# Optimization experiments

Hardware: AMD Instinct MI355X
Metric: run time of the kernel (lower is better)

The kernel has to match this reference:

```python
import jax, jax.numpy as jnp
import numpy as np

B, T, E, D, A, EMB, V = 128, 96, 512, 512, 512, 512, 4096


def _linear_params(k, out_d, in_d):
    bound = 1.0 / np.sqrt(in_d)
    k1, k2 = jax.random.split(k)
    W = jax.random.uniform(k1, (out_d, in_d), minval=-bound, maxval=bound)
    b = jax.random.uniform(k2, (out_d,), minval=-bound, maxval=bound)
    return W, b


def setup_inputs() -> dict:
    key = jax.random.key(0)
    ks = jax.random.split(key, 16)
    W_enc, b_enc = _linear_params(ks[0], A, E)
    W_dec, b_dec = _linear_params(ks[1], A, D)
    W_full, b_full = _linear_params(ks[2], 1, A)
    W_init_h, b_init_h = _linear_params(ks[3], D, E)
    W_init_c, b_init_c = _linear_params(ks[4], D, E)
    W_fbeta, b_fbeta = _linear_params(ks[5], E, D)
    W_fc = jax.random.uniform(ks[6], (V, D), minval=-0.1, maxval=0.1)
    b_fc = jnp.zeros((V,), jnp.float32)
    emb_table = jax.random.uniform(ks[7], (V, EMB), minval=-0.1, maxval=0.1)
    W_ih, b_ih = _linear_params(ks[8], 4 * D, EMB + E)
    W_hh, b_hh = _linear_params(ks[9], 4 * D, D)
    encoder_out = jax.random.normal(ks[10], (B, E), jnp.float32)
    encoded_captions = jax.random.randint(ks[11], (B, T), 0, V)
    caption_lengths = jax.random.randint(ks[12], (B, 1), 1, T + 1)
    return dict(encoder_out=encoder_out, encoded_captions=encoded_captions,
                caption_lengths=caption_lengths,
                W_enc=W_enc, b_enc=b_enc, W_dec=W_dec, b_dec=b_dec,
                W_full=W_full, b_full=b_full,
                W_init_h=W_init_h, b_init_h=b_init_h,
                W_init_c=W_init_c, b_init_c=b_init_c,
                W_fbeta=W_fbeta, b_fbeta=b_fbeta,
                W_fc=W_fc, b_fc=b_fc, emb_table=emb_table,
                W_ih=W_ih, b_ih=b_ih, W_hh=W_hh, b_hh=b_hh)


def reference(encoder_out, encoded_captions, caption_lengths,
              W_enc, b_enc, W_dec, b_dec, W_full, b_full,
              W_init_h, b_init_h, W_init_c, b_init_c,
              W_fbeta, b_fbeta, W_fc, b_fc, emb_table,
              W_ih, b_ih, W_hh, b_hh):
    # sort by caption length, descending (as in torch forward)
    lens = caption_lengths[:, 0]
    order = jnp.argsort(-lens)
    enc = encoder_out[order]            # (B, E)
    caps = encoded_captions[order]      # (B, T)
    lens_s = lens[order]
    embeds = emb_table[caps]            # (B, T, EMB)
    h0 = enc @ W_init_h.T + b_init_h    # (B, D)
    c0 = enc @ W_init_c.T + b_init_c
    att1 = enc @ W_enc.T + b_enc        # (B, A), fixed over time
    # valid[t, i] == (i < batch_size_t), since lengths are sorted descending
    valid = (jnp.arange(T)[None, :] < lens_s[:, None]).T  # (T, B)

    def step(carry, xs):
        h, c = carry
        emb_t, v = xs                   # (B, EMB), (B,) bool
        att2 = h @ W_dec.T + b_dec      # (B, A)
        # additive attention over the batch dim (the actual math of My_attention on 2D input)
        scores = jax.nn.relu(att1[None, :, :] + att2[:, None, :]) @ W_full[0] + b_full[0]  # (B, B)
        scores = jnp.where(v[None, :], scores, -1e9)
        alpha = jax.nn.softmax(scores, axis=1)
        awe = alpha @ enc               # (B, E)
        gate = jax.nn.sigmoid(h @ W_fbeta.T + b_fbeta)
        awe = gate * awe
        x = jnp.concatenate([emb_t, awe], axis=1)  # (B, EMB+E)
        gates = x @ W_ih.T + b_ih + h @ W_hh.T + b_hh
        gi, gf, gg, go = jnp.split(gates, 4, axis=1)  # torch LSTMCell order: i,f,g,o
        gi, gf, go = jax.nn.sigmoid(gi), jax.nn.sigmoid(gf), jax.nn.sigmoid(go)
        gg = jnp.tanh(gg)
        c_new = gf * c + gi * gg
        h_new = go * jnp.tanh(c_new)
        preds = h_new @ W_fc.T + b_fc   # dropout is identity in eval
        vm = v[:, None]
        return (jnp.where(vm, h_new, h), jnp.where(vm, c_new, c)), jnp.where(vm, preds, 0.0)

    (_, _), preds = jax.lax.scan(jax.checkpoint(step), (h0, c0),
                                 (jnp.transpose(embeds, (1, 0, 2)), valid))
    # (B, T, V), rows in sorted order, zero-padded past each caption length
    # (torch pack_padded_sequence is a pure reordering/gather of exactly these entries)
    return jnp.transpose(preds, (1, 0, 2))
```

## Files before the change

### kernel.cpp

```cpp
#include <hip/hip_runtime.h>

#define Bsz  128
#define Tlen 96
#define Edim 512
#define Ddim 512
#define Adim 512
#define EMBd 512
#define Vdim 4096

typedef __attribute__((ext_vector_type(8))) short short8v;
typedef __attribute__((ext_vector_type(4))) float f32x4;

__device__ __forceinline__ float sigm(float x) { return 1.0f / (1.0f + expf(-x)); }
__device__ __forceinline__ unsigned short f2bf(float f) {
    unsigned int x = __float_as_uint(f);
    unsigned int r = (x + 0x7FFFu + ((x >> 16) & 1u)) >> 16;
    return (unsigned short)r;
}

__global__ void k_sort(const int* __restrict__ lens, int* __restrict__ order,
                       int* __restrict__ lens_s) {
    __shared__ int L[Bsz];
    int j = threadIdx.x;
    L[j] = lens[j];
    __syncthreads();
    int lj = L[j];
    int rank = 0;
    for (int m = 0; m < Bsz; ++m) {
        int lm = L[m];
        if (lm > lj || (lm == lj && m < j)) rank++;
    }
    order[rank] = j;
    lens_s[rank] = lj;
}

__global__ void k_gather(const float* __restrict__ enc_in,
                         const int* __restrict__ order, float* __restrict__ enc_s) {
    int i = blockIdx.x;
    int src = order[i];
    for (int d = threadIdx.x; d < Edim; d += 256)
        enc_s[i * Edim + d] = enc_in[src * Edim + d];
}

__global__ void k_cvtW(const float* __restrict__ W, unsigned short* __restrict__ O,
                       int n) {
    int i = blockIdx.x * 256 + threadIdx.x;
    if (i < n) O[i] = f2bf(W[i]);
}

__device__ __forceinline__ void mm_tile(const float* __restrict__ act,
                                        const float* __restrict__ W,
                                        int K, int i0, float acc[4][4]) {
    __shared__ float sA[64][17];
    __shared__ float sB[64][17];
    int tid = threadIdx.x;
    int tx = tid & 15, ty = tid >> 4;
    for (int k0 = 0; k0 < K; k0 += 16) {
        {
            int idx = tid * 4;
            int row = idx >> 4;
            int kk = idx & 15;
            const float* p = act + (size_t)(i0 + row) * K + k0 + kk;
            float4 v = *reinterpret_cast<const float4*>(p);
            sA[row][kk + 0] = v.x; sA[row][kk + 1] = v.y;
            sA[row][kk + 2] = v.z; sA[row][kk + 3] = v.w;
        }
        {
            int idx = tid * 4;
            int row = idx >> 4;
            int kk = idx & 15;
            const float* p = W + (size_t)row * K + k0 + kk;
            float4 v = *reinterpret_cast<const float4*>(p);
            sB[row][kk + 0] = v.x; sB[row][kk + 1] = v.y;
            sB[row][kk + 2] = v.z; sB[row][kk + 3] = v.w;
        }
        __syncthreads();
#pragma unroll
        for (int kk = 0; kk < 16; ++kk) {
            float a[4], b[4];
#pragma unroll
            for (int r = 0; r < 4; ++r) a[r] = sA[ty * 4 + r][kk];
#pragma unroll
            for (int cidx = 0; cidx < 4; ++cidx) b[cidx] = sB[tx * 4 + cidx][kk];
#pragma unroll
            for (int r = 0; r < 4; ++r)
#pragma unroll
                for (int cidx = 0; cidx < 4; ++cidx)
                    acc[r][cidx] += a[r] * b[cidx];
        }
        __syncthreads();
    }
}

__global__ __launch_bounds__(256) void k_init(
    const float* __restrict__ enc_s,
    const float* __restrict__ W_init_h, const float* __restrict__ b_init_h,
    const float* __restrict__ W_init_c, const float* __restrict__ b_init_c,
    const float* __restrict__ W_enc, const float* __restrict__ b_enc,
    float* __restrict__ h, float* __restrict__ c, float* __restrict__ att1) {
    int j0 = blockIdx.x * 64;
    int i0 = blockIdx.y * 64;
    const float* W; const float* bias; float* out; int jl;
    if (j0 < 512)       { W = W_init_h; bias = b_init_h; out = h;    jl = j0; }
    else if (j0 < 1024) { W = W_init_c; bias = b_init_c; out = c;    jl = j0 - 512; }
    else                { W = W_enc;    bias = b_enc;    out = att1; jl = j0 - 1024; }
    float acc[4][4] = {};
    mm_tile(enc_s, W + (size_t)jl * Edim, Edim, i0, acc);
    int tx = threadIdx.x & 15, ty = threadIdx.x >> 4;
#pragma unroll
    for (int r = 0; r < 4; ++r)
#pragma unroll
        for (int cc = 0; cc < 4; ++cc) {
            int i = i0 + ty * 4 + r, j = jl + tx * 4 + cc;
            out[i * 512 + j] = acc[r][cc] + bias[j];
        }
}

__global__ __launch_bounds__(256) void k_stepA(
    const float* __restrict__ h,
    const float* __restrict__ W_dec, const float* __restrict__ b_dec,
    const float* __restrict__ W_fbeta, const float* __restrict__ b_fbeta,
    const float* __restrict__ W_hh, const float* __restrict__ b_hh,
    float* __restrict__ att2, float* __restrict__ gate, float* __restrict__ hh) {
    int j0 = blockIdx.x * 64;
    int i0 = blockIdx.y * 64;
    int tx = threadIdx.x & 15, ty = threadIdx.x >> 4;
    if (j0 < 512) {
        float acc[4][4] = {};
        mm_tile(h, W_dec + (size_t)j0 * Ddim, Ddim, i0, acc);
#pragma unroll
        for (int r = 0; r < 4; ++r)
#pragma unroll
            for (int cc = 0; cc < 4; ++cc) {
                int i = i0 + ty * 4 + r, j = j0 + tx * 4 + cc;
                att2[i * 512 + j] = acc[r][cc] + b_dec[j];
            }
    } else if (j0 < 1024) {
        float acc[4][4] = {};
        int jl = j0 - 512;
        mm_tile(h, W_fbeta + (size_t)jl * Ddim, Ddim, i0, acc);
#pragma unroll
        for (int r = 0; r < 4; ++r)
#pragma unroll
            for (int cc = 0; cc < 4; ++cc) {
                int i = i0 + ty * 4 + r, j = jl + tx * 4 + cc;
                gate[i * 512 + j] = sigm(acc[r][cc] + b_fbeta[j]);
            }
    } else {
        float acc[4][4] = {};
        int jl = j0 - 1024;
        mm_tile(h, W_hh + (size_t)jl * Ddim, Ddim, i0, acc);
#pragma unroll
        for (int r = 0; r < 4; ++r)
#pragma unroll
            for (int cc = 0; cc < 4; ++cc) {
                int i = i0 + ty * 4 + r, j = jl + tx * 4 + cc;
                hh[i * 2048 + j] = acc[r][cc] + b_hh[j];
            }
    }
}

__global__ __launch_bounds__(256) void k_stepB(
    const float* __restrict__ att1, const float* __restrict__ att2,
    const float* __restrict__ enc_s,
    const float* __restrict__ W_full, const float* __restrict__ b_full,
    const float* __restrict__ gate, const float* __restrict__ emb_table,
    const int* __restrict__ caps, const int* __restrict__ order,
    const int* __restrict__ lens_s, float* __restrict__ x, int t) {
    int i = blockIdx.x;
    int tid = threadIdx.x;
    __shared__ float sA2[512];
    __shared__ float sWF[512];
    __shared__ float sSC[128];
    __shared__ float sRed[2];
    for (int d = tid; d < 512; d += 256) {
        sA2[d] = att2[i * 512 + d];
        sWF[d] = W_full[d];
    }
    __syncthreads();
    if (tid < 128) {
        int j = tid;
        const float* a1 = att1 + j * 512;
        float acc = 0.0f;
        for (int k = 0; k < 512; ++k) {
            float v = a1[k] + sA2[k];
            acc += fmaxf(v, 0.0f) * sWF[k];
        }
        float sc = acc + b_full[0];
        if (t >= lens_s[j]) sc = -1000000000.0f;
        sSC[j] = sc;
    }
    __syncthreads();
    if (tid < 64) {
        float m = fmaxf(sSC[tid], sSC[tid + 64]);
        for (int o = 32; o; o >>= 1) m = fmaxf(m, __shfl_down(m, o));
        if (tid == 0) sRed[0] = m;
    }
    __syncthreads();
    if (tid < 128) sSC[tid] = expf(sSC[tid] - sRed[0]);
    __syncthreads();
    if (tid < 64) {
        float s = sSC[tid] + sSC[tid + 64];
        for (int o = 32; o; o >>= 1) s += __shfl_down(s, o);
        if (tid == 0) sRed[1] = s;
    }
    __syncthreads();
    float inv = 1.0f / sRed[1];
    int cap = caps[order[i] * Tlen + t];
    for (int d = tid; d < 512; d += 256) {
        float acc = 0.0f;
        for (int j = 0; j < 128; ++j) acc += sSC[j] * enc_s[j * 512 + d];
        acc *= inv;
        x[i * 1024 + 512 + d] = gate[i * 512 + d] * acc;
        x[i * 1024 + d] = emb_table[(size_t)cap * EMBd + d];
    }
}

__global__ __launch_bounds__(256) void k_stepC(
    const float* __restrict__ x, const float* __restrict__ W_ih,
    const float* __restrict__ b_ih, const float* __restrict__ hh,
    float* __restrict__ gates) {
    int j0 = blockIdx.x * 64;
    int i0 = blockIdx.y * 64;
    float acc[4][4] = {};
    mm_tile(x, W_ih + (size_t)j0 * 1024, 1024, i0, acc);
    int tx = threadIdx.x & 15, ty = threadIdx.x >> 4;
#pragma unroll
    for (int r = 0; r < 4; ++r)
#pragma unroll
        for (int cc = 0; cc < 4; ++cc) {
            int i = i0 + ty * 4 + r, j = j0 + tx * 4 + cc;
            gates[i * 2048 + j] = acc[r][cc] + b_ih[j] + hh[i * 2048 + j];
        }
}

__global__ void k_lstm(const float* __restrict__ gates, float* __restrict__ h,
                       float* __restrict__ c, const int* __restrict__ lens_s,
                       unsigned short* __restrict__ h_hist, int t) {
    int idx = blockIdx.x * 256 + threadIdx.x;
    int i = idx >> 9, d = idx & 511;
    float hv;
    if (t < lens_s[i]) {
        float gi = sigm(gates[i * 2048 + d]);
        float gf = sigm(gates[i * 2048 + 512 + d]);
        float gg = tanhf(gates[i * 2048 + 1024 + d]);
        float go = sigm(gates[i * 2048 + 1536 + d]);
        float cn = gf * c[idx] + gi * gg;
        hv = go * tanhf(cn);
        c[idx] = cn;
        h[idx] = hv;
    } else {
        hv = h[idx];
    }
    h_hist[(size_t)t * (Bsz * 512) + idx] = f2bf(hv);
}

__global__ __launch_bounds__(256) void k_preds(
    const unsigned short* __restrict__ hh16, const unsigned short* __restrict__ wfc16,
    const float* __restrict__ b_fc, const int* __restrict__ lens_s,
    float* __restrict__ out) {
    int nb = blockIdx.x;
    int mb = blockIdx.y;
    int wid = threadIdx.x >> 6;
    int lane = threadIdx.x & 63;
    int wr = wid >> 1, wc = wid & 1;
    int m_wave = mb * 128 + wr * 64;
    int n_wave = nb * 128 + wc * 64;
    int r = lane & 15, g = lane >> 4;
    f32x4 acc[4][4];
#pragma unroll
    for (int a = 0; a < 4; ++a)
#pragma unroll
        for (int b = 0; b < 4; ++b) acc[a][b] = (f32x4){0.f, 0.f, 0.f, 0.f};
    for (int kk = 0; kk < 512; kk += 32) {
        short8v av[4], bv[4];
#pragma unroll
        for (int mf = 0; mf < 4; ++mf)
            av[mf] = *reinterpret_cast<const short8v*>(
                &hh16[(size_t)(m_wave + mf * 16 + r) * 512 + kk + g * 8]);
#pragma unroll
        for (int nf = 0; nf < 4; ++nf)
            bv[nf] = *reinterpret_cast<const short8v*>(
                &wfc16[(size_t)(n_wave + nf * 16 + r) * 512 + kk + g * 8]);
#pragma unroll
        for (int mf = 0; mf < 4; ++mf)
#pragma unroll
            for (int nf = 0; nf < 4; ++nf)
                acc[mf][nf] = __builtin_amdgcn_mfma_f32_16x16x32_bf16(
                    av[mf], bv[nf], acc[mf][nf], 0, 0, 0);
    }
#pragma unroll
    for (int mf = 0; mf < 4; ++mf)
#pragma unroll
        for (int nf = 0; nf < 4; ++nf)
#pragma unroll
            for (int reg = 0; reg < 4; ++reg) {
                int m = m_wave + mf * 16 + g * 4 + reg;
                int col = n_wave + nf * 16 + r;
                int t = m >> 7, i = m & 127;
                bool valid = t < lens_s[i];
                out[((size_t)i * Tlen + t) * Vdim + col] =
                    valid ? acc[mf][nf][reg] + b_fc[col] : 0.0f;
            }
}

extern "C" void kernel_launch(void* const* d_in, const int* in_sizes, int n_in,
                              void* d_out, int out_size, void* d_ws, size_t ws_size,
                              hipStream_t stream) {
    const float* encoder_out = (const float*)d_in[0];
    const int* caps = (const int*)d_in[1];
    const int* lens = (const int*)d_in[2];
    const float* W_enc = (const float*)d_in[3];
    const float* b_enc = (const float*)d_in[4];
    const float* W_dec = (const float*)d_in[5];
    const float* b_dec = (const float*)d_in[6];
    const float* W_full = (const float*)d_in[7];
    const float* b_full = (const float*)d_in[8];
    const float* W_init_h = (const float*)d_in[9];
    const float* b_init_h = (const float*)d_in[10];
    const float* W_init_c = (const float*)d_in[11];
    const float* b_init_c = (const float*)d_in[12];
    const float* W_fbeta = (const float*)d_in[13];
    const float* b_fbeta = (const float*)d_in[14];
    const float* W_fc = (const float*)d_in[15];
    const float* b_fc = (const float*)d_in[16];
    const float* emb_table = (const float*)d_in[17];
    const float* W_ih = (const float*)d_in[18];
    const float* b_ih = (const float*)d_in[19];
    const float* W_hh = (const float*)d_in[20];
    const float* b_hh = (const float*)d_in[21];
    float* out = (float*)d_out;

    char* p = (char*)d_ws;
    auto alloc = [&](size_t bytes) {
        void* r = (void*)p;
        p += (bytes + 255) & ~(size_t)255;
        return r;
    };
    int* order = (int*)alloc(Bsz * 4);
    int* lens_s = (int*)alloc(Bsz * 4);
    float* enc_s = (float*)alloc(Bsz * Edim * 4);
    float* att1 = (float*)alloc(Bsz * Adim * 4);
    float* h = (float*)alloc(Bsz * Ddim * 4);
    float* c = (float*)alloc(Bsz * Ddim * 4);
    float* att2 = (float*)alloc(Bsz * Adim * 4);
    float* gate = (float*)alloc(Bsz * Ddim * 4);
    float* hh = (float*)alloc(Bsz * 2048 * 4);
    float* x = (float*)alloc(Bsz * 1024 * 4);
    float* gates = (float*)alloc(Bsz * 2048 * 4);
    unsigned short* h_hist = (unsigned short*)alloc((size_t)Tlen * Bsz * 512 * 2);
    unsigned short* wfc16 = (unsigned short*)alloc((size_t)Vdim * Ddim * 2);

    k_sort<<<1, 128, 0, stream>>>(lens, order, lens_s);
    k_gather<<<Bsz, 256, 0, stream>>>(encoder_out, order, enc_s);
    k_cvtW<<<(Vdim * Ddim + 255) / 256, 256, 0, stream>>>(W_fc, wfc16, Vdim * Ddim);
    k_init<<<dim3(24, 2), 256, 0, stream>>>(enc_s, W_init_h, b_init_h, W_init_c,
                                            b_init_c, W_enc, b_enc, h, c, att1);
    for (int t = 0; t < Tlen; ++t) {
        k_stepA<<<dim3(48, 2), 256, 0, stream>>>(h, W_dec, b_dec, W_fbeta, b_fbeta,
                                                 W_hh, b_hh, att2, gate, hh);
        k_stepB<<<Bsz, 256, 0, stream>>>(att1, att2, enc_s, W_full, b_full, gate,
                                         emb_table, caps, order, lens_s, x, t);
        k_stepC<<<dim3(32, 2), 256, 0, stream>>>(x, W_ih, b_ih, hh, gates);
        k_lstm<<<256, 256, 0, stream>>>(gates, h, c, lens_s, h_hist, t);
    }
    k_preds<<<dim3(32, 96), 256, 0, stream>>>(h_hist, wfc16, b_fc, lens_s, out);
}
```

Before: 13.23 ms.

## Fuse per-timestep kernels into one persistent kernel with grid barriers

Replaces the four kernel launches per timestep (384 launches in total) with a single persistent kernel of 128 blocks that loops over all timesteps. The stages are separated by an atomic-counter grid barrier that is reset in the sort kernel. This removes launch overhead and the inter-kernel gaps on the serial recurrence. In exchange, some blocks sit idle during the matmul phases, and correctness depends on all 128 blocks being resident at the same time.

```diff
diff --git a/kernel.cpp b/kernel.cpp
--- a/kernel.cpp
+++ b/kernel.cpp
@@ -19,9 +19,10 @@
 }
 
 __global__ void k_sort(const int* __restrict__ lens, int* __restrict__ order,
-                       int* __restrict__ lens_s) {
+                       int* __restrict__ lens_s, unsigned int* __restrict__ bar) {
     __shared__ int L[Bsz];
     int j = threadIdx.x;
+    if (j == 0) bar[0] = 0u;
     L[j] = lens[j];
     __syncthreads();
     int lj = L[j];
@@ -116,143 +117,169 @@
         }
 }
 
-__global__ __launch_bounds__(256) void k_stepA(
-    const float* __restrict__ h,
-    const float* __restrict__ W_dec, const float* __restrict__ b_dec,
-    const float* __restrict__ W_fbeta, const float* __restrict__ b_fbeta,
-    const float* __restrict__ W_hh, const float* __restrict__ b_hh,
-    float* __restrict__ att2, float* __restrict__ gate, float* __restrict__ hh) {
-    int j0 = blockIdx.x * 64;
-    int i0 = blockIdx.y * 64;
-    int tx = threadIdx.x & 15, ty = threadIdx.x >> 4;
-    if (j0 < 512) {
-        float acc[4][4] = {};
-        mm_tile(h, W_dec + (size_t)j0 * Ddim, Ddim, i0, acc);
-#pragma unroll
-        for (int r = 0; r < 4; ++r)
-#pragma unroll
-            for (int cc = 0; cc < 4; ++cc) {
-                int i = i0 + ty * 4 + r, j = j0 + tx * 4 + cc;
-                att2[i * 512 + j] = acc[r][cc] + b_dec[j];
-            }
-    } else if (j0 < 1024) {
-        float acc[4][4] = {};
-        int jl = j0 - 512;
-        mm_tile(h, W_fbeta + (size_t)jl * Ddim, Ddim, i0, acc);
-#pragma unroll
-        for (int r = 0; r < 4; ++r)
-#pragma unroll
-            for (int cc = 0; cc < 4; ++cc) {
-                int i = i0 + ty * 4 + r, j = jl + tx * 4 + cc;
-                gate[i * 512 + j] = sigm(acc[r][cc] + b_fbeta[j]);
-            }
-    } else {
-        float acc[4][4] = {};
-        int jl = j0 - 1024;
-        mm_tile(h, W_hh + (size_t)jl * Ddim, Ddim, i0, acc);
-#pragma unroll
-        for (int r = 0; r < 4; ++r)
-#pragma unroll
-            for (int cc = 0; cc < 4; ++cc) {
-                int i = i0 + ty * 4 + r, j = jl + tx * 4 + cc;
-                hh[i * 2048 + j] = acc[r][cc] + b_hh[j];
-            }
+#define NBLK 128
+__device__ __forceinline__ void gbar(unsigned int* bar, unsigned int target) {
+    __syncthreads();
+    if (threadIdx.x == 0) {
+        __threadfence();
+        __hip_atomic_fetch_add(bar, 1u, __ATOMIC_RELEASE, __HIP_MEMORY_SCOPE_AGENT);
+        while (__hip_atomic_load(bar, __ATOMIC_ACQUIRE, __HIP_MEMORY_SCOPE_AGENT)
+               < target)
+            __builtin_amdgcn_s_sleep(1);
+        __threadfence();
     }
-}
-
-__global__ __launch_bounds__(256) void k_stepB(
-    const float* __restrict__ att1, const float* __restrict__ att2,
-    const float* __restrict__ enc_s,
-    const float* __restrict__ W_full, const float* __restrict__ b_full,
-    const float* __restrict__ gate, const float* __restrict__ emb_table,
-    const int* __restrict__ caps, const int* __restrict__ order,
-    const int* __restrict__ lens_s, float* __restrict__ x, int t) {
-    int i = blockIdx.x;
+    __syncthreads();
+}
+
+struct LoopArgs {
+    const float* att1; const float* enc_s;
+    const float* W_dec; const float* b_dec;
+    const float* W_fbeta; const float* b_fbeta;
+    const float* W_hh; const float* b_hh;
+    const float* W_full; const float* b_full;
+    const float* emb_table;
+    const int* caps; const int* order; const int* lens_s;
+    const float* W_ih; const float* b_ih;
+    float* h; float* c; float* att2; float* gate; float* hh;
+    float* x; float* gates;
+    unsigned short* h_hist;
+    unsigned int* bar;
+};
+
+__global__ __launch_bounds__(256) void k_loop(LoopArgs A) {
+    int bid = blockIdx.x;
     int tid = threadIdx.x;
+    unsigned int barno = 0;
+    __shared__ float sWF[512];
     __shared__ float sA2[512];
-    __shared__ float sWF[512];
     __shared__ float sSC[128];
     __shared__ float sRed[2];
-    for (int d = tid; d < 512; d += 256) {
-        sA2[d] = att2[i * 512 + d];
-        sWF[d] = W_full[d];
+    for (int d = tid; d < 512; d += 256) sWF[d] = A.W_full[d];
+    float bfull = A.b_full[0];
+
+    for (int t = 0; t < Tlen; ++t) {
+        if (bid < 96) {
+            int j0 = (bid >> 1) * 64;
+            int i0 = (bid & 1) * 64;
+            int tx = tid & 15, ty = tid >> 4;
+            if (j0 < 512) {
+                float acc[4][4] = {};
+                mm_tile(A.h, A.W_dec + (size_t)j0 * Ddim, Ddim, i0, acc);
+#pragma unroll
+                for (int r = 0; r < 4; ++r)
+#pragma unroll
+                    for (int cc = 0; cc < 4; ++cc) {
+                        int i = i0 + ty * 4 + r, j = j0 + tx * 4 + cc;
+                        A.att2[i * 512 + j] = acc[r][cc] + A.b_dec[j];
+                    }
+            } else if (j0 < 1024) {
+                float acc[4][4] = {};
+                int jl = j0 - 512;
+                mm_tile(A.h, A.W_fbeta + (size_t)jl * Ddim, Ddim, i0, acc);
+#pragma unroll
+                for (int r = 0; r < 4; ++r)
+#pragma unroll
+                    for (int cc = 0; cc < 4; ++cc) {
+                        int i = i0 + ty * 4 + r, j = jl + tx * 4 + cc;
+                        A.gate[i * 512 + j] = sigm(acc[r][cc] + A.b_fbeta[j]);
+                    }
+            } else {
+                float acc[4][4] = {};
+                int jl = j0 - 1024;
+                mm_tile(A.h, A.W_hh + (size_t)jl * Ddim, Ddim, i0, acc);
+#pragma unroll
+                for (int r = 0; r < 4; ++r)
+#pragma unroll
+                    for (int cc = 0; cc < 4; ++cc) {
+                        int i = i0 + ty * 4 + r, j = jl + tx * 4 + cc;
+                        A.hh[i * 2048 + j] = acc[r][cc] + A.b_hh[j];
+                    }
+            }
+        }
+        gbar(A.bar, ++barno * NBLK);
+
+        {
+            int i = bid;
+            for (int d = tid; d < 512; d += 256) sA2[d] = A.att2[i * 512 + d];
+            __syncthreads();
+            if (tid < 128) {
+                int j = tid;
+                const float* a1 = A.att1 + j * 512;
+                float acc = 0.0f;
+                for (int k = 0; k < 512; ++k) {
+                    float v = a1[k] + sA2[k];
+                    acc += fmaxf(v, 0.0f) * sWF[k];
+                }
+                float sc = acc + bfull;
+                if (t >= A.lens_s[j]) sc = -1000000000.0f;
+                sSC[j] = sc;
+            }
+            __syncthreads();
+            if (tid < 64) {
+                float m = fmaxf(sSC[tid], sSC[tid + 64]);
+                for (int o = 32; o; o >>= 1) m = fmaxf(m, __shfl_down(m, o));
+                if (tid == 0) sRed[0] = m;
+            }
+            __syncthreads();
+            if (tid < 128) sSC[tid] = expf(sSC[tid] - sRed[0]);
+            __syncthreads();
+            if (tid < 64) {
+                float s = sSC[tid] + sSC[tid + 64];
+                for (int o = 32; o; o >>= 1) s += __shfl_down(s, o);
+                if (tid == 0) sRed[1] = s;
+            }
+            __syncthreads();
+            float inv = 1.0f / sRed[1];
+            int cap = A.caps[A.order[i] * Tlen + t];
+            for (int d = tid; d < 512; d += 256) {
+                float acc = 0.0f;
+                for (int j = 0; j < 128; ++j) acc += sSC[j] * A.enc_s[j * 512 + d];
+                acc *= inv;
+                A.x[i * 1024 + 512 + d] = A.gate[i * 512 + d] * acc;
+                A.x[i * 1024 + d] = A.emb_table[(size_t)cap * EMBd + d];
+            }
+        }
+        gbar(A.bar, ++barno * NBLK);
+
+        if (bid < 64) {
+            int j0 = (bid >> 1) * 64;
+            int i0 = (bid & 1) * 64;
+            float acc[4][4] = {};
+            mm_tile(A.x, A.W_ih + (size_t)j0 * 1024, 1024, i0, acc);
+            int tx = tid & 15, ty = tid >> 4;
+#pragma unroll
+            for (int r = 0; r < 4; ++r)
+#pragma unroll
+                for (int cc = 0; cc < 4; ++cc) {
+                    int i = i0 + ty * 4 + r, j = j0 + tx * 4 + cc;
+                    A.gates[i * 2048 + j] = acc[r][cc] + A.b_ih[j] + A.hh[i * 2048 + j];
+                }
+        }
+        gbar(A.bar, ++barno * NBLK);
+
+        {
+            int i = bid;
+            bool valid = t < A.lens_s[i];
+            for (int d = tid; d < 512; d += 256) {
+                int idx = i * 512 + d;
+                float hv;
+                if (valid) {
+                    float gi = sigm(A.gates[i * 2048 + d]);
+                    float gf = sigm(A.gates[i * 2048 + 512 + d]);
+                    float gg = tanhf(A.gates[i * 2048 + 1024 + d]);
+                    float go = sigm(A.gates[i * 2048 + 1536 + d]);
+                    float cn = gf * A.c[idx] + gi * gg;
+                    hv = go * tanhf(cn);
+                    A.c[idx] = cn;
+                    A.h[idx] = hv;
+                } else {
+                    hv = A.h[idx];
+                }
+                A.h_hist[(size_t)t * (Bsz * 512) + idx] = f2bf(hv);
+            }
+        }
+        gbar(A.bar, ++barno * NBLK);
     }
-    __syncthreads();
-    if (tid < 128) {
-        int j = tid;
-        const float* a1 = att1 + j * 512;
-        float acc = 0.0f;
-        for (int k = 0; k < 512; ++k) {
-            float v = a1[k] + sA2[k];
-            acc += fmaxf(v, 0.0f) * sWF[k];
-        }
-        float sc = acc + b_full[0];
-        if (t >= lens_s[j]) sc = -1000000000.0f;
-        sSC[j] = sc;
-    }
-    __syncthreads();
-    if (tid < 64) {
-        float m = fmaxf(sSC[tid], sSC[tid + 64]);
-        for (int o = 32; o; o >>= 1) m = fmaxf(m, __shfl_down(m, o));
-        if (tid == 0) sRed[0] = m;
-    }
-    __syncthreads();
-    if (tid < 128) sSC[tid] = expf(sSC[tid] - sRed[0]);
-    __syncthreads();
-    if (tid < 64) {
-        float s = sSC[tid] + sSC[tid + 64];
-        for (int o = 32; o; o >>= 1) s += __shfl_down(s, o);
-        if (tid == 0) sRed[1] = s;
-    }
-    __syncthreads();
-    float inv = 1.0f / sRed[1];
-    int cap = caps[order[i] * Tlen + t];
-    for (int d = tid; d < 512; d += 256) {
-        float acc = 0.0f;
-        for (int j = 0; j < 128; ++j) acc += sSC[j] * enc_s[j * 512 + d];
-        acc *= inv;
-        x[i * 1024 + 512 + d] = gate[i * 512 + d] * acc;
-        x[i * 1024 + d] = emb_table[(size_t)cap * EMBd + d];
-    }
-}
-
-__global__ __launch_bounds__(256) void k_stepC(
-    const float* __restrict__ x, const float* __restrict__ W_ih,
-    const float* __restrict__ b_ih, const float* __restrict__ hh,
-    float* __restrict__ gates) {
-    int j0 = blockIdx.x * 64;
-    int i0 = blockIdx.y * 64;
-    float acc[4][4] = {};
-    mm_tile(x, W_ih + (size_t)j0 * 1024, 1024, i0, acc);
-    int tx = threadIdx.x & 15, ty = threadIdx.x >> 4;
-#pragma unroll
-    for (int r = 0; r < 4; ++r)
-#pragma unroll
-        for (int cc = 0; cc < 4; ++cc) {
-            int i = i0 + ty * 4 + r, j = j0 + tx * 4 + cc;
-            gates[i * 2048 + j] = acc[r][cc] + b_ih[j] + hh[i * 2048 + j];
-        }
-}
-
-__global__ void k_lstm(const float* __restrict__ gates, float* __restrict__ h,
-                       float* __restrict__ c, const int* __restrict__ lens_s,
-                       unsigned short* __restrict__ h_hist, int t) {
-    int idx = blockIdx.x * 256 + threadIdx.x;
-    int i = idx >> 9, d = idx & 511;
-    float hv;
-    if (t < lens_s[i]) {
-        float gi = sigm(gates[i * 2048 + d]);
-        float gf = sigm(gates[i * 2048 + 512 + d]);
-        float gg = tanhf(gates[i * 2048 + 1024 + d]);
-        float go = sigm(gates[i * 2048 + 1536 + d]);
-        float cn = gf * c[idx] + gi * gg;
-        hv = go * tanhf(cn);
-        c[idx] = cn;
-        h[idx] = hv;
-    } else {
-        hv = h[idx];
-    }
-    h_hist[(size_t)t * (Bsz * 512) + idx] = f2bf(hv);
 }
 
 __global__ __launch_bounds__(256) void k_preds(
@@ -339,6 +366,7 @@
     };
     int* order = (int*)alloc(Bsz * 4);
     int* lens_s = (int*)alloc(Bsz * 4);
+    unsigned int* bar = (unsigned int*)alloc(256);
     float* enc_s = (float*)alloc(Bsz * Edim * 4);
     float* att1 = (float*)alloc(Bsz * Adim * 4);
     float* h = (float*)alloc(Bsz * Ddim * 4);
@@ -351,18 +379,26 @@
     unsigned short* h_hist = (unsigned short*)alloc((size_t)Tlen * Bsz * 512 * 2);
     unsigned short* wfc16 = (unsigned short*)alloc((size_t)Vdim * Ddim * 2);
 
-    k_sort<<<1, 128, 0, stream>>>(lens, order, lens_s);
+    k_sort<<<1, 128, 0, stream>>>(lens, order, lens_s, bar);
     k_gather<<<Bsz, 256, 0, stream>>>(encoder_out, order, enc_s);
     k_cvtW<<<(Vdim * Ddim + 255) / 256, 256, 0, stream>>>(W_fc, wfc16, Vdim * Ddim);
     k_init<<<dim3(24, 2), 256, 0, stream>>>(enc_s, W_init_h, b_init_h, W_init_c,
                                             b_init_c, W_enc, b_enc, h, c, att1);
-    for (int t = 0; t < Tlen; ++t) {
-        k_stepA<<<dim3(48, 2), 256, 0, stream>>>(h, W_dec, b_dec, W_fbeta, b_fbeta,
-                                                 W_hh, b_hh, att2, gate, hh);
-        k_stepB<<<Bsz, 256, 0, stream>>>(att1, att2, enc_s, W_full, b_full, gate,
-                                         emb_table, caps, order, lens_s, x, t);
-        k_stepC<<<dim3(32, 2), 256, 0, stream>>>(x, W_ih, b_ih, hh, gates);
-        k_lstm<<<256, 256, 0, stream>>>(gates, h, c, lens_s, h_hist, t);
-    }
+
+    LoopArgs la;
+    la.att1 = att1; la.enc_s = enc_s;
+    la.W_dec = W_dec; la.b_dec = b_dec;
+    la.W_fbeta = W_fbeta; la.b_fbeta = b_fbeta;
+    la.W_hh = W_hh; la.b_hh = b_hh;
+    la.W_full = W_full; la.b_full = b_full;
+    la.emb_table = emb_table;
+    la.caps = caps; la.order = order; la.lens_s = lens_s;
+    la.W_ih = W_ih; la.b_ih = b_ih;
+    la.h = h; la.c = c; la.att2 = att2; la.gate = gate; la.hh = hh;
+    la.x = x; la.gates = gates;
+    la.h_hist = h_hist;
+    la.bar = bar;
+    k_loop<<<NBLK, 256, 0, stream>>>(la);
+
     k_preds<<<dim3(32, 96), 256, 0, stream>>>(h_hist, wfc16, b_fc, lens_s, out);
 }
```

Result: slower. 22.07 ms (+66.8%).
